# Kernel tuning notes

Hardware: AMD Instinct MI355X
Metric: run time of the kernel (lower is better)

Reference implementation:

```python
import jax, jax.numpy as jnp
import numpy as np


def setup_inputs() -> dict:
    key = jax.random.key(0)
    B, N, C = 16, 4096, 768  # SAM ViT-B token tensor [batch, tokens, channels]
    x = jax.random.normal(key, (B, N, C), dtype=jnp.float32)
    k = 384        # int(C * p2) with p2 = 0.5
    largest = 1    # torch.topk largest=True
    return {"x": x, "k": k, "largest": largest}


def reference(x, k, largest):
    # torch.topk(x, k, dim=2, largest=largest) with dim=2 == last axis for 3D x,
    # then scatter values back into zeros_like(x) at the selected indices.
    if largest:
        vals, idx = jax.lax.top_k(x, k)            # [B, N, k]
    else:
        neg_vals, idx = jax.lax.top_k(-x, k)
        vals = -neg_vals
    B, N, _ = x.shape
    b = jnp.arange(B)[:, None, None]               # broadcast batch index
    n = jnp.arange(N)[None, :, None]               # broadcast token index
    out = jnp.zeros_like(x).at[b, n, idx].set(vals)
    return out
```

## Files before the change

kernel.cpp:

```cpp
#include <hip/hip_runtime.h>
#include <cstdint>


constexpr int C    = 768;
constexpr int TPB  = 256;
constexpr int WPB  = TPB / 64;
constexpr int EPL  = C / 64;
constexpr int NV   = EPL / 4;

__device__ __forceinline__ uint32_t f2key(float f, uint32_t flip) {
    uint32_t b = __float_as_uint(f);
    uint32_t u = (b & 0x80000000u) ? ~b : (b | 0x80000000u);
    return u ^ flip;
}

__global__ __launch_bounds__(TPB) void topk_scatter_row(
        const float* __restrict__ x,
        const int*   __restrict__ pk,
        const int*   __restrict__ plg,
        float*       __restrict__ out,
        int rows) {
    __shared__ int hist_all[WPB][256];

    const int lane = threadIdx.x & 63;
    const int wid  = threadIdx.x >> 6;
    const int row  = blockIdx.x * WPB + wid;
    if (row >= rows) return;

    int* hist = hist_all[wid];

    const float* xr   = x   + (size_t)row * C;
    float*       orow = out + (size_t)row * C;

    const int      k    = pk[0];
    const uint32_t flip = (plg[0] != 0) ? 0u : 0xFFFFFFFFu;

    float    v[EPL];
    uint32_t key[EPL];
    #pragma unroll
    for (int j = 0; j < NV; ++j) {
        float4 t = ((const float4*)xr)[j * 64 + lane];
        v[j*4+0] = t.x; v[j*4+1] = t.y; v[j*4+2] = t.z; v[j*4+3] = t.w;
    }
    #pragma unroll
    for (int e = 0; e < EPL; ++e) key[e] = f2key(v[e], flip);

    if (k <= 0) {
        #pragma unroll
        for (int j = 0; j < NV; ++j)
            ((float4*)orow)[j * 64 + lane] = make_float4(0.f, 0.f, 0.f, 0.f);
        return;
    }

    uint32_t prefix = 0;
    int      kk     = k;
    int      shift  = 24;
    bool     need_tie = false;

    for (int r = 0; r < 4; ++r) {
        ((int4*)hist)[lane] = make_int4(0, 0, 0, 0);

        const uint32_t pmask = (r == 0) ? 0u : ~((1u << (shift + 8)) - 1u);
        #pragma unroll
        for (int e = 0; e < EPL; ++e) {
            if (((key[e] ^ prefix) & pmask) == 0)
                atomicAdd(&hist[(key[e] >> shift) & 255u], 1);
        }

        int4 b = ((const int4*)hist)[lane];
        int t0 = b.x + b.y + b.z + b.w;

        int s = t0;
        #pragma unroll
        for (int off = 1; off < 64; off <<= 1) {
            int o = __shfl_down(s, off);
            s += (lane + off < 64) ? o : 0;
        }
        const int upper = s - t0;

        int ge[4];
        ge[3] = upper + b.w;
        ge[2] = ge[3] + b.z;
        ge[1] = ge[2] + b.y;
        ge[0] = ge[1] + b.x;
        const int bins[4] = { b.x, b.y, b.z, b.w };

        int found_d = -1, found_gt = 0, found_bc = 0;
        #pragma unroll
        for (int i = 0; i < 4; ++i) {
            int gt = ge[i] - bins[i];
            if (gt < kk && kk <= ge[i]) {
                found_d = lane * 4 + i; found_gt = gt; found_bc = bins[i];
            }
        }
        unsigned long long m = __ballot(found_d >= 0);
        int src = __ffsll((long long)m) - 1;
        int d  = __shfl(found_d, src);
        int gt = __shfl(found_gt, src);
        int bc = __shfl(found_bc, src);

        kk -= gt;
        prefix |= ((uint32_t)d) << shift;

        if (kk == bc) break;
        if (shift == 0) { need_tie = true; break; }
        shift -= 8;
    }

    uint32_t selmask = 0;
    if (need_tie) {
        int base = 0;
        #pragma unroll
        for (int j = 0; j < NV; ++j) {
            int eq[4], le = 0;
            #pragma unroll
            for (int c = 0; c < 4; ++c) { eq[c] = (key[j*4+c] == prefix) ? 1 : 0; le += eq[c]; }
            int p = le;
            #pragma unroll
            for (int off = 1; off < 64; off <<= 1) {
                int o = __shfl_up(p, off);
                p += (lane >= off) ? o : 0;
            }
            const int excl = p - le;
            const int tot  = __shfl(p, 63);
            int acc = base + excl;
            #pragma unroll
            for (int c = 0; c < 4; ++c) {
                if (eq[c] && acc < kk) selmask |= 1u << (j*4+c);
                acc += eq[c];
            }
            base += tot;
        }
    }

    #pragma unroll
    for (int j = 0; j < NV; ++j) {
        float4 o;
        float* oo = (float*)&o;
        #pragma unroll
        for (int c = 0; c < 4; ++c) {
            const int e = j*4 + c;
            bool sel = need_tie ? ((key[e] > prefix) || ((selmask >> e) & 1u))
                                : (key[e] >= prefix);
            oo[c] = sel ? v[e] : 0.0f;
        }
        ((float4*)orow)[j * 64 + lane] = o;
    }
}

extern "C" void kernel_launch(void* const* d_in, const int* in_sizes, int n_in,
                              void* d_out, int out_size, void* d_ws, size_t ws_size,
                              hipStream_t stream) {
    const float* x   = (const float*)d_in[0];
    const int*   pk  = (const int*)d_in[1];
    const int*   plg = (const int*)d_in[2];
    float*       out = (float*)d_out;

    const int rows   = in_sizes[0] / C;
    const int blocks = (rows + WPB - 1) / WPB;
    topk_scatter_row<<<blocks, TPB, 0, stream>>>(x, pk, plg, out, rows);
}
```

Baseline: 337.5 us.

## Replace LDS histogram radix select with bitwise ballot/popcount radix select

Swaps the four-pass, 8-bit radix select for a bit-by-bit binary search over the key. The old version built a 256-bin histogram per pass with LDS atomics and then did a wavefront prefix scan. The new one counts candidates at each bit with wavefront ballots and popcount, and exits early once the count matches k exactly. This removes LDS atomic contention and the scans, but the loop can run up to 32 iterations of 12 ballots each.

```diff
diff --git a/kernel.cpp b/kernel.cpp
--- a/kernel.cpp
+++ b/kernel.cpp
@@ -20,14 +20,10 @@
         const int*   __restrict__ plg,
         float*       __restrict__ out,
         int rows) {
-    __shared__ int hist_all[WPB][256];
-
     const int lane = threadIdx.x & 63;
     const int wid  = threadIdx.x >> 6;
     const int row  = blockIdx.x * WPB + wid;
     if (row >= rows) return;
-
-    int* hist = hist_all[wid];
 
     const float* xr   = x   + (size_t)row * C;
     float*       orow = out + (size_t)row * C;
@@ -52,63 +48,32 @@
         return;
     }
 
-    uint32_t prefix = 0;
-    int      kk     = k;
-    int      shift  = 24;
-    bool     need_tie = false;
+    uint32_t prefix  = 0;
+    int      kk      = k;
+    int      candcnt = C;
+    bool     done    = false;
 
-    for (int r = 0; r < 4; ++r) {
-        ((int4*)hist)[lane] = make_int4(0, 0, 0, 0);
+    for (int b = 31; b >= 0; --b) {
+        const uint32_t pw  = prefix | (1u << b);
+        const uint32_t lim = 1u << b;
+        int cnt = 0;
+        #pragma unroll
+        for (int e = 0; e < EPL; ++e)
+            cnt += __popcll(__ballot((key[e] ^ pw) < lim));
 
-        const uint32_t pmask = (r == 0) ? 0u : ~((1u << (shift + 8)) - 1u);
-        #pragma unroll
-        for (int e = 0; e < EPL; ++e) {
-            if (((key[e] ^ prefix) & pmask) == 0)
-                atomicAdd(&hist[(key[e] >> shift) & 255u], 1);
+        if (cnt >= kk) {
+            prefix  = pw;
+            candcnt = cnt;
+            if (cnt == kk) { done = true; break; }
+        } else {
+            kk      -= cnt;
+            candcnt -= cnt;
+            if (candcnt == kk) { done = true; break; }
         }
-
-        int4 b = ((const int4*)hist)[lane];
-        int t0 = b.x + b.y + b.z + b.w;
-
-        int s = t0;
-        #pragma unroll
-        for (int off = 1; off < 64; off <<= 1) {
-            int o = __shfl_down(s, off);
-            s += (lane + off < 64) ? o : 0;
-        }
-        const int upper = s - t0;
-
-        int ge[4];
-        ge[3] = upper + b.w;
-        ge[2] = ge[3] + b.z;
-        ge[1] = ge[2] + b.y;
-        ge[0] = ge[1] + b.x;
-        const int bins[4] = { b.x, b.y, b.z, b.w };
-
-        int found_d = -1, found_gt = 0, found_bc = 0;
-        #pragma unroll
-        for (int i = 0; i < 4; ++i) {
-            int gt = ge[i] - bins[i];
-            if (gt < kk && kk <= ge[i]) {
-                found_d = lane * 4 + i; found_gt = gt; found_bc = bins[i];
-            }
-        }
-        unsigned long long m = __ballot(found_d >= 0);
-        int src = __ffsll((long long)m) - 1;
-        int d  = __shfl(found_d, src);
-        int gt = __shfl(found_gt, src);
-        int bc = __shfl(found_bc, src);
-
-        kk -= gt;
-        prefix |= ((uint32_t)d) << shift;
-
-        if (kk == bc) break;
-        if (shift == 0) { need_tie = true; break; }
-        shift -= 8;
     }
 
     uint32_t selmask = 0;
-    if (need_tie) {
+    if (!done) {
         int base = 0;
         #pragma unroll
         for (int j = 0; j < NV; ++j) {
@@ -140,8 +105,8 @@
         #pragma unroll
         for (int c = 0; c < 4; ++c) {
             const int e = j*4 + c;
-            bool sel = need_tie ? ((key[e] > prefix) || ((selmask >> e) & 1u))
-                                : (key[e] >= prefix);
+            bool sel = done ? (key[e] >= prefix)
+                            : ((key[e] > prefix) || ((selmask >> e) & 1u));
             oo[c] = sel ? v[e] : 0.0f;
         }
         ((float4*)orow)[j * 64 + lane] = o;
```

Measured after the change: 340.2 us. Within noise of the previous version (+0.8%).
